# Kernel tuning notes

Measured on AMD Instinct MI355X. Metric: run time of the kernel, lower is better.

The kernel has to match this reference:

```python
import jax, jax.numpy as jnp
import numpy as np
from jax import lax

B, T, I, H = 64, 512, 512, 512


def setup_inputs() -> dict:
    key = jax.random.key(0)
    ks = jax.random.split(key, 9)
    s_in = 1.0 / np.sqrt(I)
    s_h = 1.0 / np.sqrt(H)
    return {
        "x": jax.random.normal(ks[0], (B, T, I), dtype=jnp.float32),
        "h0_f": jnp.zeros((B, H), dtype=jnp.float32),
        "h0_b": jnp.zeros((B, H), dtype=jnp.float32),
        # cell_f params (torch Linear: y = x @ W.T + b)
        "Wxf_w": jax.random.uniform(ks[1], (H, I), jnp.float32, -s_in, s_in),
        "Wxf_b": jax.random.uniform(ks[2], (H,), jnp.float32, -s_in, s_in),
        "Whf_w": jax.random.uniform(ks[3], (H, H), jnp.float32, -s_h, s_h),
        # cell_b params
        "Wxb_w": jax.random.uniform(ks[4], (H, I), jnp.float32, -s_in, s_in),
        "Wxb_b": jax.random.uniform(ks[5], (H,), jnp.float32, -s_in, s_in),
        "Whb_w": jax.random.uniform(ks[6], (H, H), jnp.float32, -s_h, s_h),
    }


def _run_dir(x_tbi, h0, Wx_w, Wx_b, Wh_w, reverse):
    # Precompute input projections as one big GEMM (same math as per-step Linear)
    xproj = jnp.einsum("tbi,hi->tbh", x_tbi, Wx_w) + Wx_b  # (T,B,H)

    def step(h, xp):
        h = jnp.tanh(xp + h @ Wh_w.T)
        return h, h

    hT, hs = lax.scan(step, h0, xproj, reverse=reverse)
    return hT, hs  # hs in natural time order even when reverse=True


def reference(x, h0_f, h0_b, Wxf_w, Wxf_b, Whf_w, Wxb_w, Wxb_b, Whb_w):
    x_tbi = jnp.transpose(x, (1, 0, 2))  # (T,B,I)
    hT_f, hs_f = _run_dir(x_tbi, h0_f, Wxf_w, Wxf_b, Whf_w, reverse=False)
    hT_b, hs_b = _run_dir(x_tbi, h0_b, Wxb_w, Wxb_b, Whb_w, reverse=True)
    y = jnp.concatenate([hs_f, hs_b], axis=-1)  # (T,B,2H)
    y = jnp.transpose(y, (1, 0, 2))  # (B,T,2H)
    return y, hT_f, hT_b
```

## Files before the change

kernel.cpp:

```cpp
#include <hip/hip_runtime.h>

#define T_LEN 512
#define B_SZ  64
#define I_SZ  512
#define H_SZ  512

using half8   = __attribute__((ext_vector_type(8))) _Float16;
using half4   = __attribute__((ext_vector_type(4))) _Float16;
using float4v = __attribute__((ext_vector_type(4))) float;

__device__ __forceinline__ float fast_tanh(float x) {
    float e = __expf(2.0f * x);
    return 1.0f - 2.0f * __builtin_amdgcn_rcpf(e + 1.0f);
}

__global__ __launch_bounds__(512) void xproj_kernel(
    const float* __restrict__ x,
    const float* __restrict__ Wf, const float* __restrict__ bf,
    const float* __restrict__ Wb, const float* __restrict__ bb,
    _Float16* __restrict__ xp)
{
    __shared__ _Float16 Ash[16384];
    __shared__ _Float16 Bsh[16384];

    const int bid = blockIdx.x;
    const int swz = (bid & 7) * 64 + (bid >> 3);
    const int dir = swz & 1;
    const int nb  = (swz >> 1) & 1;
    const int mb  = swz >> 2;
    const int m0  = mb * 256;
    const int n0  = nb * 256;

    const float* __restrict__ W    = dir ? Wb : Wf;
    const float* __restrict__ bias = dir ? bb : bf;

    const int tid  = threadIdx.x;
    const int wv   = tid >> 6;
    const int lane = tid & 63;
    const int lm   = lane & 15;
    const int lq   = lane >> 4;
    const int wm   = wv >> 2;
    const int wn   = wv & 3;

    int rowA[4], ldsA[4];
    #pragma unroll
    for (int r = 0; r < 4; r++) {
        const int q   = r*512 + tid;
        const int row = q >> 3;
        const int khi = q & 7;
        rowA[r] = row;
        ldsA[r] = (row >> 4)*1024 + (khi*16 + ((row & 15) ^ khi))*8;
    }

    float4v acc[8][4];
    #pragma unroll
    for (int mt = 0; mt < 8; mt++)
        #pragma unroll
        for (int nt = 0; nt < 4; nt++)
            acc[mt][nt] = (float4v){0,0,0,0};

    for (int k0 = 0; k0 < I_SZ; k0 += 64) {
        float4v st[16];
        #pragma unroll
        for (int r = 0; r < 4; r++) {
            const int q   = r*512 + tid;
            const int khi = q & 7;
            const float* ga = x + (size_t)(m0 + rowA[r])*I_SZ + k0 + khi*8;
            const float* gb = W + (size_t)(n0 + rowA[r])*I_SZ + k0 + khi*8;
            st[r*2]     = *(const float4v*)ga;
            st[r*2 + 1] = *(const float4v*)(ga + 4);
            st[8 + r*2]     = *(const float4v*)gb;
            st[8 + r*2 + 1] = *(const float4v*)(gb + 4);
        }
        __syncthreads();
        #pragma unroll
        for (int r = 0; r < 4; r++) {
            half8 va, vb;
            #pragma unroll
            for (int e = 0; e < 4; e++) {
                va[e]   = (_Float16)st[r*2][e];
                va[e+4] = (_Float16)st[r*2+1][e];
                vb[e]   = (_Float16)st[8+r*2][e];
                vb[e+4] = (_Float16)st[8+r*2+1][e];
            }
            *(half8*)&Ash[ldsA[r]] = va;
            *(half8*)&Bsh[ldsA[r]] = vb;
        }
        __syncthreads();

        #pragma unroll
        for (int ks = 0; ks < 2; ks++) {
            const int khi = ks*4 + lq;
            const int go  = (khi*16 + (lm ^ khi))*8;
            half8 bfr[4];
            #pragma unroll
            for (int nt = 0; nt < 4; nt++)
                bfr[nt] = *(const half8*)&Bsh[(wn*4 + nt)*1024 + go];
            #pragma unroll
            for (int mt = 0; mt < 8; mt++) {
                half8 afr = *(const half8*)&Ash[(wm*8 + mt)*1024 + go];
                #pragma unroll
                for (int nt = 0; nt < 4; nt++)
                    acc[mt][nt] = __builtin_amdgcn_mfma_f32_16x16x32_f16(
                        afr, bfr[nt], acc[mt][nt], 0, 0, 0);
            }
        }
    }

    #pragma unroll
    for (int nt = 0; nt < 4; nt++) {
        const int n  = n0 + wn*64 + nt*16 + lm;
        const float bv = bias[n];
        #pragma unroll
        for (int mt = 0; mt < 8; mt++) {
            #pragma unroll
            for (int j = 0; j < 4; j++) {
                const int m = m0 + wm*128 + mt*16 + lq*4 + j;
                const int b = m >> 9;
                const int t = m & 511;
                xp[(((size_t)dir*T_LEN + t)*B_SZ + b)*H_SZ + n] =
                    (_Float16)(acc[mt][nt][j] + bv);
            }
        }
    }
}

__global__ __launch_bounds__(512, 2) void rnn_kernel(
    const _Float16* __restrict__ xp,
    const float* __restrict__ Whf, const float* __restrict__ Whb,
    const float* __restrict__ h0f, const float* __restrict__ h0b,
    float* __restrict__ out)
{
    const int blk  = blockIdx.x;
    const int dir  = blk >> 2;
    const int b0   = (blk & 3) * 16;
    const int tid  = threadIdx.x;
    const int wv   = tid >> 6;
    const int lane = tid & 63;
    const int lq   = lane >> 4;
    const int lm   = lane & 15;

    const float* __restrict__ Wh = dir ? Whb : Whf;
    const float* __restrict__ h0 = dir ? h0b : h0f;

    __shared__ _Float16 hl[2][8192];
    __shared__ _Float16 wl[8][16][64][8];

    half8 bw[4][12];
    {
        const float* wr0 = Wh + ((size_t)(wv*64 + lm*4)) * H_SZ + lq*8;
        #pragma unroll
        for (int nt = 0; nt < 4; nt++) {
            const float* wr = wr0 + (size_t)nt * H_SZ;
            #pragma unroll
            for (int kt = 0; kt < 16; kt++) {
                float4v lo = *(const float4v*)(wr + kt*32);
                float4v hi = *(const float4v*)(wr + kt*32 + 4);
                half8 v;
                #pragma unroll
                for (int e = 0; e < 4; e++) { v[e] = (_Float16)lo[e]; v[e+4] = (_Float16)hi[e]; }
                if (kt < 12) bw[nt][kt] = v;
                else *(half8*)&wl[wv][nt*4 + (kt - 12)][lane][0] = v;
            }
        }
    }

    #pragma unroll
    for (int r = 0; r < 2; r++) {
        const int gi  = r*512 + tid;
        const int khi = gi >> 4;
        const int b   = gi & 15;
        const float* p = h0 + (size_t)(b0 + b)*H_SZ + khi*8;
        half8 v;
        #pragma unroll
        for (int e = 0; e < 8; e++) v[e] = (_Float16)p[e];
        *(half8*)&hl[0][(khi*16 + (b ^ (khi & 15))) * 8] = v;
    }
    __syncthreads();

    const _Float16* wlp = &wl[wv][0][lane][0];

    const int ts = dir ? -1 : 1;
    const int t0 = dir ? (T_LEN - 1) : 0;
    const _Float16* xpt = xp + (((size_t)dir*T_LEN + t0)*B_SZ + (b0 + lq*4))*H_SZ
                             + wv*64 + lm*4;
    const ptrdiff_t xstep = (ptrdiff_t)ts * (B_SZ * H_SZ);
    float* yb = out + ((size_t)(b0 + lq*4)*T_LEN + t0)*1024 + dir*512 + wv*64 + lm*4;
    const ptrdiff_t ystep = (ptrdiff_t)ts * 1024;

    const int khiw = wv*8 + (lm >> 1);
    const int gofs = (lm & 1) * 4;

    half4 xq[4];
    #pragma unroll
    for (int j = 0; j < 4; j++) xq[j] = *(const half4*)(xpt + j*H_SZ);

    #pragma unroll 1
    for (int s = 0; s < T_LEN; s++) {
        const _Float16* hr = hl[s & 1];
        _Float16*       hw = hl[(s & 1) ^ 1];

        float4v acc[4];
        #pragma unroll
        for (int nt = 0; nt < 4; nt++)
            #pragma unroll
            for (int j = 0; j < 4; j++)
                acc[nt][j] = (float)xq[j][nt];

        if (s + 1 < T_LEN) {
            xpt += xstep;
            #pragma unroll
            for (int j = 0; j < 4; j++) xq[j] = *(const half4*)(xpt + j*H_SZ);
        }

        #pragma unroll
        for (int g = 0; g < 3; g++) {
            half8 af[4];
            #pragma unroll
            for (int i = 0; i < 4; i++) {
                const int c = (g*4 + i)*4 + lq;
                af[i] = *(const half8*)&hr[(c*16 + (lm ^ (c & 15))) * 8];
            }
            #pragma unroll
            for (int i = 0; i < 4; i++)
                #pragma unroll
                for (int nt = 0; nt < 4; nt++)
                    acc[nt] = __builtin_amdgcn_mfma_f32_16x16x32_f16(af[i], bw[nt][g*4 + i], acc[nt], 0, 0, 0);
        }
        {
            half8 af[4];
            #pragma unroll
            for (int i = 0; i < 4; i++) {
                const int c = (12 + i)*4 + lq;
                af[i] = *(const half8*)&hr[(c*16 + (lm ^ (c & 15))) * 8];
            }
            #pragma unroll
            for (int i = 0; i < 4; i++)
                #pragma unroll
                for (int nt = 0; nt < 4; nt++) {
                    half8 w = *(const half8*)(wlp + (nt*4 + i)*512);
                    acc[nt] = __builtin_amdgcn_mfma_f32_16x16x32_f16(af[i], w, acc[nt], 0, 0, 0);
                }
        }

        #pragma unroll
        for (int j = 0; j < 4; j++) {
            float4v v;
            #pragma unroll
            for (int nt = 0; nt < 4; nt++) v[nt] = fast_tanh(acc[nt][j]);
            half4 pk;
            #pragma unroll
            for (int nt = 0; nt < 4; nt++) pk[nt] = (_Float16)v[nt];
            *(half4*)&hw[(khiw*16 + ((lq*4 + j) ^ (khiw & 15))) * 8 + gofs] = pk;
            __builtin_nontemporal_store(v, (float4v*)(yb + (size_t)j*(T_LEN*1024)));
            if (s == T_LEN - 1) {
                float* hp = out + 33554432 + (size_t)dir*32768
                          + (size_t)(b0 + lq*4 + j)*H_SZ + wv*64 + lm*4;
                __builtin_nontemporal_store(v, (float4v*)hp);
            }
        }
        yb += ystep;

        asm volatile("s_waitcnt lgkmcnt(0)" ::: "memory");
        __builtin_amdgcn_s_barrier();
        __builtin_amdgcn_sched_barrier(0);
    }
}

extern "C" void kernel_launch(void* const* d_in, const int* in_sizes, int n_in,
                              void* d_out, int out_size, void* d_ws, size_t ws_size,
                              hipStream_t stream) {
    const float* x   = (const float*)d_in[0];
    const float* h0f = (const float*)d_in[1];
    const float* h0b = (const float*)d_in[2];
    const float* Wxf = (const float*)d_in[3];
    const float* bxf = (const float*)d_in[4];
    const float* Whf = (const float*)d_in[5];
    const float* Wxb = (const float*)d_in[6];
    const float* bxb = (const float*)d_in[7];
    const float* Whb = (const float*)d_in[8];
    float* out = (float*)d_out;

    _Float16* xpb = (_Float16*)d_ws;

    hipLaunchKernelGGL(xproj_kernel, dim3(512), dim3(512), 0, stream,
                       x, Wxf, bxf, Wxb, bxb, xpb);
    hipLaunchKernelGGL(rnn_kernel, dim3(8), dim3(512), 0, stream,
                       xpb, Whf, Whb, h0f, h0b, out);
}
```

Measured before the change: 1.741 ms.

## Fuse input projection GEMM and recurrence into one kernel with per-chunk flags

Merges the input-projection GEMM and the recurrent kernel into a single launch. Eight blocks run the recurrence while the other blocks compute projection tiles in time order; each tile bumps an atomic counter that the recurrence waits on before reading that time chunk. The goal is to overlap the projection GEMM with the serial scan instead of running them back to back. To fit the shared-memory budget, the hidden state drops from double to single buffering, which adds a second barrier on every recurrence step and so risks slowing the serial loop.

```diff
diff --git a/kernel.cpp b/kernel.cpp
--- a/kernel.cpp
+++ b/kernel.cpp
@@ -14,137 +14,139 @@
     return 1.0f - 2.0f * __builtin_amdgcn_rcpf(e + 1.0f);
 }
 
-__global__ __launch_bounds__(512) void xproj_kernel(
+__global__ __launch_bounds__(512, 2) void fused_kernel(
     const float* __restrict__ x,
-    const float* __restrict__ Wf, const float* __restrict__ bf,
-    const float* __restrict__ Wb, const float* __restrict__ bb,
-    _Float16* __restrict__ xp)
+    const float* __restrict__ Wxf, const float* __restrict__ bxf,
+    const float* __restrict__ Whf,
+    const float* __restrict__ Wxb, const float* __restrict__ bxb,
+    const float* __restrict__ Whb,
+    const float* __restrict__ h0f, const float* __restrict__ h0b,
+    _Float16* __restrict__ xp,
+    float* __restrict__ out,
+    unsigned int* __restrict__ cnt)
 {
-    __shared__ _Float16 Ash[16384];
-    __shared__ _Float16 Bsh[16384];
-
-    const int bid = blockIdx.x;
-    const int swz = (bid & 7) * 64 + (bid >> 3);
-    const int dir = swz & 1;
-    const int nb  = (swz >> 1) & 1;
-    const int mb  = swz >> 2;
-    const int m0  = mb * 256;
-    const int n0  = nb * 256;
-
-    const float* __restrict__ W    = dir ? Wb : Wf;
-    const float* __restrict__ bias = dir ? bb : bf;
+    __shared__ _Float16 smem[73728];
 
     const int tid  = threadIdx.x;
     const int wv   = tid >> 6;
     const int lane = tid & 63;
     const int lm   = lane & 15;
     const int lq   = lane >> 4;
-    const int wm   = wv >> 2;
-    const int wn   = wv & 3;
-
-    int rowA[4], ldsA[4];
-    #pragma unroll
-    for (int r = 0; r < 4; r++) {
-        const int q   = r*512 + tid;
-        const int row = q >> 3;
-        const int khi = q & 7;
-        rowA[r] = row;
-        ldsA[r] = (row >> 4)*1024 + (khi*16 + ((row & 15) ^ khi))*8;
-    }
-
-    float4v acc[8][4];
-    #pragma unroll
-    for (int mt = 0; mt < 8; mt++)
-        #pragma unroll
-        for (int nt = 0; nt < 4; nt++)
-            acc[mt][nt] = (float4v){0,0,0,0};
-
-    for (int k0 = 0; k0 < I_SZ; k0 += 64) {
-        float4v st[16];
-        #pragma unroll
-        for (int r = 0; r < 4; r++) {
-            const int q   = r*512 + tid;
-            const int khi = q & 7;
-            const float* ga = x + (size_t)(m0 + rowA[r])*I_SZ + k0 + khi*8;
-            const float* gb = W + (size_t)(n0 + rowA[r])*I_SZ + k0 + khi*8;
-            st[r*2]     = *(const float4v*)ga;
-            st[r*2 + 1] = *(const float4v*)(ga + 4);
-            st[8 + r*2]     = *(const float4v*)gb;
-            st[8 + r*2 + 1] = *(const float4v*)(gb + 4);
-        }
+
+    if (blockIdx.x >= 8) {
+        const int xb  = blockIdx.x - 8;
+        const int ord = xb >> 2;
+        const int sub = xb & 3;
+        const int dir = sub & 1;
+        const int nb  = sub >> 1;
+        const int ts4 = dir ? (127 - ord) : ord;
+        const int n0  = nb * 256;
+
+        const float* __restrict__ W    = dir ? Wxb : Wxf;
+        const float* __restrict__ bias = dir ? bxb : bxf;
+
+        _Float16* Ash = smem;
+        _Float16* Bsh = smem + 16384;
+
+        const int wm = wv >> 2;
+        const int wn = wv & 3;
+
+        float4v acc[8][4];
+        #pragma unroll
+        for (int mt = 0; mt < 8; mt++)
+            #pragma unroll
+            for (int nt = 0; nt < 4; nt++)
+                acc[mt][nt] = (float4v){0,0,0,0};
+
+        for (int k0 = 0; k0 < I_SZ; k0 += 64) {
+            float4v st[16];
+            #pragma unroll
+            for (int rr = 0; rr < 4; rr++) {
+                const int q   = rr*512 + tid;
+                const int row = q >> 3;
+                const int khi = q & 7;
+                const int bb  = row >> 2;
+                const int tt  = ts4*4 + (row & 3);
+                const float* ga = x + ((size_t)bb*T_LEN + tt)*I_SZ + k0 + khi*8;
+                const float* gb = W + (size_t)(n0 + row)*I_SZ + k0 + khi*8;
+                st[rr*2]       = *(const float4v*)ga;
+                st[rr*2 + 1]   = *(const float4v*)(ga + 4);
+                st[8 + rr*2]   = *(const float4v*)gb;
+                st[8 + rr*2+1] = *(const float4v*)(gb + 4);
+            }
+            __syncthreads();
+            #pragma unroll
+            for (int rr = 0; rr < 4; rr++) {
+                const int q   = rr*512 + tid;
+                const int row = q >> 3;
+                const int khi = q & 7;
+                const int lo_ = (row >> 4)*1024 + (khi*16 + ((row & 15) ^ khi))*8;
+                half8 va, vb;
+                #pragma unroll
+                for (int e = 0; e < 4; e++) {
+                    va[e]   = (_Float16)st[rr*2][e];
+                    va[e+4] = (_Float16)st[rr*2+1][e];
+                    vb[e]   = (_Float16)st[8+rr*2][e];
+                    vb[e+4] = (_Float16)st[8+rr*2+1][e];
+                }
+                *(half8*)&Ash[lo_] = va;
+                *(half8*)&Bsh[lo_] = vb;
+            }
+            __syncthreads();
+
+            #pragma unroll
+            for (int ks = 0; ks < 2; ks++) {
+                const int khi = ks*4 + lq;
+                const int go  = (khi*16 + (lm ^ khi))*8;
+                half8 bfr[4];
+                #pragma unroll
+                for (int nt = 0; nt < 4; nt++)
+                    bfr[nt] = *(const half8*)&Bsh[(wn*4 + nt)*1024 + go];
+                #pragma unroll
+                for (int mt = 0; mt < 8; mt++) {
+                    half8 afr = *(const half8*)&Ash[(wm*8 + mt)*1024 + go];
+                    #pragma unroll
+                    for (int nt = 0; nt < 4; nt++)
+                        acc[mt][nt] = __builtin_amdgcn_mfma_f32_16x16x32_f16(
+                            afr, bfr[nt], acc[mt][nt], 0, 0, 0);
+                }
+            }
+        }
+
+        #pragma unroll
+        for (int nt = 0; nt < 4; nt++) {
+            const int n  = n0 + wn*64 + nt*16 + lm;
+            const float bv = bias[n];
+            #pragma unroll
+            for (int mt = 0; mt < 8; mt++) {
+                #pragma unroll
+                for (int j = 0; j < 4; j++) {
+                    const int row = wm*128 + mt*16 + lq*4 + j;
+                    const int bb  = row >> 2;
+                    const int tt  = ts4*4 + (row & 3);
+                    xp[(((size_t)dir*T_LEN + tt)*B_SZ + bb)*H_SZ + n] =
+                        (_Float16)(acc[mt][nt][j] + bv);
+                }
+            }
+        }
+
+        asm volatile("s_waitcnt vmcnt(0)" ::: "memory");
         __syncthreads();
-        #pragma unroll
-        for (int r = 0; r < 4; r++) {
-            half8 va, vb;
-            #pragma unroll
-            for (int e = 0; e < 4; e++) {
-                va[e]   = (_Float16)st[r*2][e];
-                va[e+4] = (_Float16)st[r*2+1][e];
-                vb[e]   = (_Float16)st[8+r*2][e];
-                vb[e+4] = (_Float16)st[8+r*2+1][e];
-            }
-            *(half8*)&Ash[ldsA[r]] = va;
-            *(half8*)&Bsh[ldsA[r]] = vb;
-        }
-        __syncthreads();
-
-        #pragma unroll
-        for (int ks = 0; ks < 2; ks++) {
-            const int khi = ks*4 + lq;
-            const int go  = (khi*16 + (lm ^ khi))*8;
-            half8 bfr[4];
-            #pragma unroll
-            for (int nt = 0; nt < 4; nt++)
-                bfr[nt] = *(const half8*)&Bsh[(wn*4 + nt)*1024 + go];
-            #pragma unroll
-            for (int mt = 0; mt < 8; mt++) {
-                half8 afr = *(const half8*)&Ash[(wm*8 + mt)*1024 + go];
-                #pragma unroll
-                for (int nt = 0; nt < 4; nt++)
-                    acc[mt][nt] = __builtin_amdgcn_mfma_f32_16x16x32_f16(
-                        afr, bfr[nt], acc[mt][nt], 0, 0, 0);
-            }
-        }
-    }
-
-    #pragma unroll
-    for (int nt = 0; nt < 4; nt++) {
-        const int n  = n0 + wn*64 + nt*16 + lm;
-        const float bv = bias[n];
-        #pragma unroll
-        for (int mt = 0; mt < 8; mt++) {
-            #pragma unroll
-            for (int j = 0; j < 4; j++) {
-                const int m = m0 + wm*128 + mt*16 + lq*4 + j;
-                const int b = m >> 9;
-                const int t = m & 511;
-                xp[(((size_t)dir*T_LEN + t)*B_SZ + b)*H_SZ + n] =
-                    (_Float16)(acc[mt][nt][j] + bv);
-            }
-        }
-    }
-}
-
-__global__ __launch_bounds__(512, 2) void rnn_kernel(
-    const _Float16* __restrict__ xp,
-    const float* __restrict__ Whf, const float* __restrict__ Whb,
-    const float* __restrict__ h0f, const float* __restrict__ h0b,
-    float* __restrict__ out)
-{
-    const int blk  = blockIdx.x;
-    const int dir  = blk >> 2;
-    const int b0   = (blk & 3) * 16;
-    const int tid  = threadIdx.x;
-    const int wv   = tid >> 6;
-    const int lane = tid & 63;
-    const int lq   = lane >> 4;
-    const int lm   = lane & 15;
+        if (tid == 0)
+            __hip_atomic_fetch_add(&cnt[dir*128 + ts4], 1u,
+                                   __ATOMIC_RELEASE, __HIP_MEMORY_SCOPE_AGENT);
+        return;
+    }
+
+    const int blk = blockIdx.x;
+    const int dir = blk >> 2;
+    const int b0  = (blk & 3) * 16;
 
     const float* __restrict__ Wh = dir ? Whb : Whf;
     const float* __restrict__ h0 = dir ? h0b : h0f;
 
-    __shared__ _Float16 hl[2][8192];
-    __shared__ _Float16 wl[8][16][64][8];
+    _Float16* hl  = smem;
+    _Float16* wlb = smem + 8192;
 
     half8 bw[4][12];
     {
@@ -160,7 +162,7 @@
                 #pragma unroll
                 for (int e = 0; e < 4; e++) { v[e] = (_Float16)lo[e]; v[e+4] = (_Float16)hi[e]; }
                 if (kt < 12) bw[nt][kt] = v;
-                else *(half8*)&wl[wv][nt*4 + (kt - 12)][lane][0] = v;
+                else *(half8*)&wlb[wv*8192 + (nt*4 + (kt - 12))*512 + lane*8] = v;
             }
         }
     }
@@ -174,11 +176,11 @@
         half8 v;
         #pragma unroll
         for (int e = 0; e < 8; e++) v[e] = (_Float16)p[e];
-        *(half8*)&hl[0][(khi*16 + (b ^ (khi & 15))) * 8] = v;
+        *(half8*)&hl[(khi*16 + (b ^ (khi & 15))) * 8] = v;
     }
     __syncthreads();
 
-    const _Float16* wlp = &wl[wv][0][lane][0];
+    const _Float16* wlp = wlb + wv*8192 + lane*8;
 
     const int ts = dir ? -1 : 1;
     const int t0 = dir ? (T_LEN - 1) : 0;
@@ -191,15 +193,20 @@
     const int khiw = wv*8 + (lm >> 1);
     const int gofs = (lm & 1) * 4;
 
+    {
+        const unsigned int* f = cnt + dir*128 + (t0 >> 2);
+        if (tid == 0)
+            while (__hip_atomic_load(f, __ATOMIC_ACQUIRE,
+                                     __HIP_MEMORY_SCOPE_AGENT) < 2u) {}
+        __syncthreads();
+    }
+
     half4 xq[4];
     #pragma unroll
     for (int j = 0; j < 4; j++) xq[j] = *(const half4*)(xpt + j*H_SZ);
 
     #pragma unroll 1
     for (int s = 0; s < T_LEN; s++) {
-        const _Float16* hr = hl[s & 1];
-        _Float16*       hw = hl[(s & 1) ^ 1];
-
         float4v acc[4];
         #pragma unroll
         for (int nt = 0; nt < 4; nt++)
@@ -208,6 +215,14 @@
                 acc[nt][j] = (float)xq[j][nt];
 
         if (s + 1 < T_LEN) {
+            const int tn = dir ? (510 - s) : (s + 1);
+            if ((tn & 3) == (dir ? 3 : 0)) {
+                const unsigned int* f = cnt + dir*128 + (tn >> 2);
+                if (tid == 0)
+                    while (__hip_atomic_load(f, __ATOMIC_ACQUIRE,
+                                             __HIP_MEMORY_SCOPE_AGENT) < 2u) {}
+                __syncthreads();
+            }
             xpt += xstep;
             #pragma unroll
             for (int j = 0; j < 4; j++) xq[j] = *(const half4*)(xpt + j*H_SZ);
@@ -219,7 +234,7 @@
             #pragma unroll
             for (int i = 0; i < 4; i++) {
                 const int c = (g*4 + i)*4 + lq;
-                af[i] = *(const half8*)&hr[(c*16 + (lm ^ (c & 15))) * 8];
+                af[i] = *(const half8*)&hl[(c*16 + (lm ^ (c & 15))) * 8];
             }
             #pragma unroll
             for (int i = 0; i < 4; i++)
@@ -232,7 +247,7 @@
             #pragma unroll
             for (int i = 0; i < 4; i++) {
                 const int c = (12 + i)*4 + lq;
-                af[i] = *(const half8*)&hr[(c*16 + (lm ^ (c & 15))) * 8];
+                af[i] = *(const half8*)&hl[(c*16 + (lm ^ (c & 15))) * 8];
             }
             #pragma unroll
             for (int i = 0; i < 4; i++)
@@ -243,27 +258,34 @@
                 }
         }
 
+        half4 pks[4];
         #pragma unroll
         for (int j = 0; j < 4; j++) {
             float4v v;
             #pragma unroll
             for (int nt = 0; nt < 4; nt++) v[nt] = fast_tanh(acc[nt][j]);
-            half4 pk;
-            #pragma unroll
-            for (int nt = 0; nt < 4; nt++) pk[nt] = (_Float16)v[nt];
-            *(half4*)&hw[(khiw*16 + ((lq*4 + j) ^ (khiw & 15))) * 8 + gofs] = pk;
             __builtin_nontemporal_store(v, (float4v*)(yb + (size_t)j*(T_LEN*1024)));
             if (s == T_LEN - 1) {
                 float* hp = out + 33554432 + (size_t)dir*32768
                           + (size_t)(b0 + lq*4 + j)*H_SZ + wv*64 + lm*4;
                 __builtin_nontemporal_store(v, (float4v*)hp);
             }
+            half4 pk;
+            #pragma unroll
+            for (int nt = 0; nt < 4; nt++) pk[nt] = (_Float16)v[nt];
+            pks[j] = pk;
         }
         yb += ystep;
 
         asm volatile("s_waitcnt lgkmcnt(0)" ::: "memory");
         __builtin_amdgcn_s_barrier();
-        __builtin_amdgcn_sched_barrier(0);
+
+        #pragma unroll
+        for (int j = 0; j < 4; j++)
+            *(half4*)&hl[(khiw*16 + ((lq*4 + j) ^ (khiw & 15))) * 8 + gofs] = pks[j];
+
+        asm volatile("s_waitcnt lgkmcnt(0)" ::: "memory");
+        __builtin_amdgcn_s_barrier();
     }
 }
 
@@ -281,10 +303,12 @@
     const float* Whb = (const float*)d_in[8];
     float* out = (float*)d_out;
 
-    _Float16* xpb = (_Float16*)d_ws;
-
-    hipLaunchKernelGGL(xproj_kernel, dim3(512), dim3(512), 0, stream,
-                       x, Wxf, bxf, Wxb, bxb, xpb);
-    hipLaunchKernelGGL(rnn_kernel, dim3(8), dim3(512), 0, stream,
-                       xpb, Whf, Whb, h0f, h0b, out);
+    _Float16*     xpb = (_Float16*)d_ws;
+    unsigned int* cnt = (unsigned int*)((char*)d_ws + 67108864);
+
+    (void)hipMemsetAsync(cnt, 0, 2 * 128 * sizeof(unsigned int), stream);
+
+    hipLaunchKernelGGL(fused_kernel, dim3(520), dim3(512), 0, stream,
+                       x, Wxf, bxf, Whf, Wxb, bxb, Whb, h0f, h0b,
+                       xpb, out, cnt);
 }
```

Measured after the change: 1.454 ms. 1.2x faster.
